# Kernel tuning notes

Measured on AMD Instinct MI355X. Metric: run time of the kernel, lower is better.

The kernel has to match this reference:

```python
import jax, jax.numpy as jnp
import numpy as np

D_MODEL = 1024
SEQ_LEN = 2048
NUM_EIGH = 24
BATCH = 4


def _spectral_filters(L, K):
    # Hankel matrix Z[i,j] = 2 / ((i+j)^3 - (i+j)), 1-indexed; top-K eigvecs scaled by sigma^0.25
    t = np.arange(1, L + 1, dtype=np.float64)
    s = t[:, None] + t[None, :]
    Z = 2.0 / (s ** 3 - s)
    sigma, phi = np.linalg.eigh(Z)
    phi_k = phi[:, -K:] * (sigma[-K:] ** 0.25)
    return jnp.asarray(phi_k, dtype=jnp.float32)


def setup_inputs() -> dict:
    key = jax.random.key(0)
    k1, k2, k3 = jax.random.split(key, 3)
    std = 1.0 / np.sqrt(D_MODEL)
    return {
        "x": jax.random.normal(k1, (BATCH, SEQ_LEN, D_MODEL), dtype=jnp.float32),
        "M_inputs": jax.random.normal(k2, (D_MODEL, D_MODEL), dtype=jnp.float32) * std,
        "M_filters": jax.random.normal(k3, (NUM_EIGH, D_MODEL), dtype=jnp.float32) * std,
        "phi": _spectral_filters(SEQ_LEN, NUM_EIGH),
    }


def _convolve_approx(u, v, n):
    # u: [B, L, D] inputs (already projected); v: [L, D] per-channel causal filters.
    # Dual-branch causal FFT convolution:
    #   plus[b,t,d]  = sum_{s<=t} v[s,d] * u[b,t-s,d]
    #   minus[b,t,d] = (-1)^t * sum_{s<=t} v[s,d] * (-1)^{t-s} u[b,t-s,d]
    B, L, D = u.shape
    sgn = jnp.where(jnp.arange(L) % 2 == 0, 1.0, -1.0).astype(u.dtype)[None, :, None]  # [1,L,1]
    V = jnp.fft.rfft(v, n=n, axis=0)                     # [F, D] complex
    U = jnp.stack([u, u * sgn], axis=-1)                 # [B, L, D, 2]
    Uf = jnp.fft.rfft(U, n=n, axis=1)                    # [B, F, D, 2]
    conv = jnp.fft.irfft(V[None, :, :, None] * Uf, n=n, axis=1)[:, :L]  # [B, L, D, 2]
    return conv[..., 0], conv[..., 1] * sgn


def reference(x, M_inputs, M_filters, phi):
    L = x.shape[1]
    n = 1 << int(np.ceil(np.log2(2 * L - 1)))  # next pow2 of 2L-1 (static)
    x_proj = x @ M_inputs                       # [B, L, D]
    phi_proj = phi[:L] @ M_filters              # [L, D]
    spectral_plus, spectral_minus = _convolve_approx(x_proj, phi_proj, n)
    return spectral_plus + spectral_minus
```

## Files before the change

### kernel.cpp

```cpp
#include <hip/hip_runtime.h>
#include <stdint.h>

#define D_MODEL 1024
#define SEQ 2048
#define HALF 1024
#define K_EIG 24
#define GUARD4 24
#define K4 128
#define K4P (GUARD4 + K4)
#define WE_JP4 72

typedef __attribute__((ext_vector_type(8))) short bf16x8;
typedef __attribute__((ext_vector_type(4))) float f32x4;
typedef _Float16 f16;
typedef _Float16 f16x2 __attribute__((ext_vector_type(2)));
typedef unsigned int uint;

#define GAS __attribute__((address_space(1)))
#define LAS __attribute__((address_space(3)))

static __device__ __forceinline__ unsigned short f2bf(float f) {
  union { float f; uint32_t u; } v; v.f = f;
  uint32_t u = v.u;
  u += 0x7FFFu + ((u >> 16) & 1u);
  return (unsigned short)(u >> 16);
}

static __device__ __forceinline__ float dot2(uint w2, uint u2, float c) {
  return __builtin_amdgcn_fdot2(__builtin_bit_cast(f16x2, w2),
                                __builtin_bit_cast(f16x2, u2), c, false);
}

static __device__ __forceinline__ uint pkrtz(float lo, float hi) {
  return __builtin_bit_cast(uint, __builtin_amdgcn_cvt_pkrtz(lo, hi));
}

static __device__ __forceinline__ uint pkbf(float lo, float hi) {
  return (uint)f2bf(lo) | ((uint)f2bf(hi) << 16);
}

__global__ __launch_bounds__(256) void k_prep(const float* __restrict__ Mi,
                                              const float* __restrict__ phi,
                                              const float* __restrict__ Mf,
                                              uint4* __restrict__ u4,
                                              unsigned short* __restrict__ Mt,
                                              uint4* __restrict__ we4) {
  __shared__ float smem[1056];
  const int blk = (int)blockIdx.x;
  const int tidx = threadIdx.x;

  if (blk < 768) {
    int r = blk / 96;
    int idx = (blk - r * 96) * 256 + tidx;
    u4[(size_t)r * (K4P * 1024) + idx] = make_uint4(0u, 0u, 0u, 0u);
    return;
  }
  if (blk < 1792) {
    int bidx = blk - 768;
    int n0 = (bidx & 31) * 32, k0 = (bidx >> 5) * 32;
    float (*tile)[33] = (float(*)[33])smem;
    int tx = tidx & 31, ty = tidx >> 5;
    #pragma unroll
    for (int r = 0; r < 32; r += 8)
      tile[ty + r][tx] = Mi[(size_t)(k0 + ty + r) * D_MODEL + n0 + tx];
    __syncthreads();
    #pragma unroll
    for (int r = 0; r < 32; r += 8)
      Mt[(size_t)(n0 + ty + r) * D_MODEL + k0 + tx] = f2bf(tile[tx][ty + r]);
    return;
  }
  {
    int bidx = blk - 1792;
    int jp4 = bidx % 72;
    int d = (bidx / 72) * 256 + tidx;
    if (jp4 >= 64) {
      we4[(size_t)jp4 * D_MODEL + d] = make_uint4(0u, 0u, 0u, 0u);
      return;
    }
    float (*ph)[K_EIG] = (float(*)[K_EIG])smem;
    if (tidx < 8 * K_EIG) {
      int s = tidx / K_EIG, k = tidx - s * K_EIG;
      ph[s][k] = phi[(size_t)(16 * jp4 + 2 * s) * K_EIG + k];
    }
    __syncthreads();
    float s[8] = {};
    #pragma unroll
    for (int k = 0; k < K_EIG; ++k) {
      float mv = Mf[(size_t)k * D_MODEL + d];
      #pragma unroll
      for (int j = 0; j < 8; ++j) s[j] = fmaf(ph[j][k], mv, s[j]);
    }
    uint4 o;
    o.x = pkrtz(2.f * s[0], 2.f * s[1]);
    o.y = pkrtz(2.f * s[2], 2.f * s[3]);
    o.z = pkrtz(2.f * s[4], 2.f * s[5]);
    o.w = pkrtz(2.f * s[6], 2.f * s[7]);
    we4[(size_t)jp4 * D_MODEL + d] = o;
  }
}

__global__ __launch_bounds__(256) void k_gemm(const float* __restrict__ X,
                                              const unsigned short* __restrict__ Bt,
                                              uint* __restrict__ Ug) {
  __shared__ float Asf[3][128 * 32];
  __shared__ unsigned short Bs[3][128 * 32];
  const int bid = (int)blockIdx.x;
  const int swz = (bid & 7) * 64 + (bid >> 3);
  const int m0 = (swz >> 3) * 128;
  const int n0 = (swz & 7) * 128;
  const int tid = threadIdx.x;
  const int lane = tid & 63;
  const int wave = tid >> 6;
  const int wm = wave >> 1, wn = wave & 1;
  const int qo = lane >> 4;

  const int a_row = lane >> 3;
  const int a_chunk = (lane & 7) ^ a_row;
  const int b_row = lane >> 2;
  const int b_chunk = (lane & 3) ^ (b_row & 3);

#define GSTAGE(buf, k0v)                                                                  \
  {                                                                                       \
    float* abase = &Asf[buf][0];                                                          \
    unsigned short* bbase = &Bs[buf][0];                                                  \
    _Pragma("unroll") for (int c = 0; c < 4; ++c) {                                       \
      int rbase = wave * 32 + c * 8;                                                      \
      const float* srcA = X + (size_t)(m0 + rbase + a_row) * 1024 + (k0v) + a_chunk * 4;  \
      __builtin_amdgcn_global_load_lds((const GAS void*)srcA,                             \
                                       (LAS void*)(abase + rbase * 32), 16, 0, 0);        \
    }                                                                                     \
    _Pragma("unroll") for (int c = 0; c < 2; ++c) {                                       \
      int rbase = wave * 32 + c * 16;                                                     \
      const unsigned short* srcB = Bt + (size_t)(n0 + rbase + b_row) * 1024 + (k0v) + b_chunk * 8; \
      __builtin_amdgcn_global_load_lds((const GAS void*)srcB,                             \
                                       (LAS void*)(bbase + rbase * 32), 16, 0, 0);        \
    }                                                                                     \
  }

  f32x4 acc[4][4] = {};

  GSTAGE(0, 0);
  GSTAGE(1, 32);

  int cur = 0;
  int nx2 = 2;
#pragma unroll 1
  for (int t = 0; t < 32; ++t) {
    if (t < 31) {
      asm volatile("s_waitcnt vmcnt(6)" ::: "memory");
    } else {
      asm volatile("s_waitcnt vmcnt(0)" ::: "memory");
    }
    __builtin_amdgcn_s_barrier();
    asm volatile("" ::: "memory");
    if (t < 30) GSTAGE(nx2, (t + 2) * 32);

    bf16x8 a[4], b[4];
    const float* Acur = &Asf[cur][0];
    const unsigned short* Bcur = &Bs[cur][0];
    #pragma unroll
    for (int mt = 0; mt < 4; ++mt) {
      int m = wm * 64 + mt * 16 + (lane & 15);
      const float* base = Acur + m * 32;
      int s0 = (2 * qo) ^ (lane & 7);
      int s1 = s0 ^ 1;
      float4 f0 = *(const float4*)(base + s0 * 4);
      float4 f1 = *(const float4*)(base + s1 * 4);
      uint4 pk;
      pk.x = pkbf(f0.x, f0.y); pk.y = pkbf(f0.z, f0.w);
      pk.z = pkbf(f1.x, f1.y); pk.w = pkbf(f1.z, f1.w);
      a[mt] = __builtin_bit_cast(bf16x8, pk);
    }
    #pragma unroll
    for (int nt = 0; nt < 4; ++nt) {
      int n = wn * 64 + nt * 16 + (lane & 15);
      int sb = qo ^ (lane & 3);
      b[nt] = *(const bf16x8*)(Bcur + n * 32 + sb * 8);
    }
    #pragma unroll
    for (int mt = 0; mt < 4; ++mt)
      #pragma unroll
      for (int nt = 0; nt < 4; ++nt)
        acc[mt][nt] = __builtin_amdgcn_mfma_f32_16x16x32_bf16(a[mt], b[nt], acc[mt][nt], 0, 0, 0);

    cur = (cur == 2) ? 0 : cur + 1;
    nx2 = (nx2 == 2) ? 0 : nx2 + 1;
  }
#undef GSTAGE

  const int crow = (lane >> 4) * 4;
  const int ccol = lane & 15;
  #pragma unroll
  for (int mt = 0; mt < 4; ++mt) {
    int m = m0 + wm * 64 + mt * 16 + crow;
    int b_ = m >> 11;
    int t0 = m & 2047;
    int r_e = b_ << 1;
    int k4 = t0 >> 4;
    int dwo = (t0 >> 2) & 3;
    size_t base_e = ((size_t)(r_e * K4P + GUARD4 + k4) * 1024) * 4 + dwo;
    size_t base_o = ((size_t)((r_e + 1) * K4P + GUARD4 + k4) * 1024) * 4 + dwo;
    #pragma unroll
    for (int nt = 0; nt < 4; ++nt) {
      int n = n0 + wn * 64 + nt * 16 + ccol;
      Ug[base_e + (size_t)n * 4] = pkrtz(acc[mt][nt][0], acc[mt][nt][2]);
      Ug[base_o + (size_t)n * 4] = pkrtz(acc[mt][nt][1], acc[mt][nt][3]);
    }
  }
}

__global__ __launch_bounds__(512, 6) void k_conv(const uint4* __restrict__ u4,
                                                 const uint4* __restrict__ we4,
                                                 float* __restrict__ out) {
  __shared__ uint4 u_r[32 * 64];
  __shared__ uint4 w_s[2][8][64];
  const int flat = blockIdx.x;
  const int dt = flat & 15;
  const int r  = (flat >> 4) & 7;
  const int a  = 7 - (flat >> 7);
  const int d0 = dt * 64;
  const int tid = threadIdx.x;
  const int dl = tid & 63;
  const int ig = tid >> 6;

  const uint4* ub = u4 + ((size_t)r * K4P + GUARD4) * 1024 + d0;
  const int b_ = r >> 1, p = r & 1;

#define STAGEU(k40)                                                                     \
  {                                                                                     \
    int k4e = (k40) + ig;                                                               \
    const uint4* src = ub + (long long)k4e * 1024 + dl;                                 \
    __builtin_amdgcn_global_load_lds((const GAS void*)src,                              \
                                     (LAS void*)(u_r + (k4e & 31) * 64), 16, 0, 0);     \
  }

#define STAGEW(ch)                                                                      \
  {                                                                                     \
    const uint4* src = we4 + (size_t)((ch) * 8 + ig) * 1024 + d0 + dl;                  \
    __builtin_amdgcn_global_load_lds((const GAS void*)src,                              \
                                     (LAS void*)(&w_s[(ch) & 1][ig][0]), 16, 0, 0);     \
  }

  const int i0 = a * 128;
  const int ibase = i0 + ig * 16;
  const int niter = (2 * a + 2) < 8 ? (2 * a + 2) : 8;

  STAGEU(16 * a - 8); STAGEU(16 * a); STAGEU(16 * a + 8);
  STAGEW(0);
  __syncthreads();

  float acc[16];
#pragma unroll
  for (int o = 0; o < 16; ++o) acc[o] = 0.f;

#pragma unroll 1
  for (int c = 0; c < niter; ++c) {
    STAGEU(16 * a - 8 * c - 16);
    STAGEW(c + 1);
    const int cb = c & 1;
    const int kbase = 16 * a + 2 * ig - 8 * c - 2;
#pragma unroll
    for (int s = 0; s < 4; ++s) {
      const int kb = kbase - 2 * s;
      uint4 v0 = u_r[((kb + 0) & 31) * 64 + dl];
      uint4 v1 = u_r[((kb + 1) & 31) * 64 + dl];
      uint4 v2 = u_r[((kb + 2) & 31) * 64 + dl];
      uint4 v3 = u_r[((kb + 3) & 31) * 64 + dl];
      uint P[16];
      P[0] = v0.x; P[1] = v0.y; P[2] = v0.z; P[3] = v0.w;
      P[4] = v1.x; P[5] = v1.y; P[6] = v1.z; P[7] = v1.w;
      P[8] = v2.x; P[9] = v2.y; P[10] = v2.z; P[11] = v2.w;
      P[12] = v3.x; P[13] = v3.y; P[14] = v3.z; P[15] = v3.w;
      uint4 wv0 = w_s[cb][2 * s][dl];
      uint4 wv1 = w_s[cb][2 * s + 1][dl];
      uint W[8];
      W[0] = wv0.x; W[1] = wv0.y; W[2] = wv0.z; W[3] = wv0.w;
      W[4] = wv1.x; W[5] = wv1.y; W[6] = wv1.z; W[7] = wv1.w;
      uint WS[8];
#pragma unroll
      for (int q = 0; q < 8; ++q) WS[q] = __builtin_amdgcn_alignbit(W[q], W[q], 16);
      uint pe[15];
#pragma unroll
      for (int j = 0; j < 15; ++j) pe[j] = __builtin_amdgcn_perm(P[j + 1], P[j], 0x03020504u);
#pragma unroll
      for (int q = 0; q < 8; ++q) {
#pragma unroll
        for (int h = 0; h < 8; ++h) {
          acc[2 * h]     = dot2(W[q],  pe[7 - q + h], acc[2 * h]);
          acc[2 * h + 1] = dot2(WS[q], P[8 - q + h],  acc[2 * h + 1]);
        }
      }
    }
    __syncthreads();
  }

#pragma unroll
  for (int o = 0; o < 16; ++o)
    out[((size_t)b_ * SEQ + 2 * (ibase + o) + p) * D_MODEL + d0 + dl] = acc[o];
#undef STAGEU
#undef STAGEW
}

extern "C" void kernel_launch(void* const* d_in, const int* in_sizes, int n_in,
                              void* d_out, int out_size, void* d_ws, size_t ws_size,
                              hipStream_t stream) {
  const float* x   = (const float*)d_in[0];
  const float* Mi  = (const float*)d_in[1];
  const float* Mf  = (const float*)d_in[2];
  const float* phi = (const float*)d_in[3];
  float* out = (float*)d_out;

  unsigned short* Mt = (unsigned short*)d_out;

  char* ws = (char*)d_ws;
  uint4* we4 = (uint4*)(ws);
  uint4* u4  = (uint4*)(ws + (2u << 20));

  hipLaunchKernelGGL(k_prep, dim3(2080), dim3(256), 0, stream, Mi, phi, Mf, u4, Mt, we4);
  hipLaunchKernelGGL(k_gemm, dim3(512), dim3(256), 0, stream, x, Mt, (uint*)u4);
  hipLaunchKernelGGL(k_conv, dim3(1024), dim3(512), 0, stream, u4, we4, out);
}
```

Baseline: 118.2 us.

## Load filter weights directly into registers with software prefetch instead of LDS

```diff
diff --git a/kernel.cpp b/kernel.cpp
--- a/kernel.cpp
+++ b/kernel.cpp
@@ -209,11 +209,10 @@
   }
 }
 
-__global__ __launch_bounds__(512, 6) void k_conv(const uint4* __restrict__ u4,
+__global__ __launch_bounds__(512, 8) void k_conv(const uint4* __restrict__ u4,
                                                  const uint4* __restrict__ we4,
                                                  float* __restrict__ out) {
   __shared__ uint4 u_r[32 * 64];
-  __shared__ uint4 w_s[2][8][64];
   const int flat = blockIdx.x;
   const int dt = flat & 15;
   const int r  = (flat >> 4) & 7;
@@ -224,6 +223,7 @@
   const int ig = tid >> 6;
 
   const uint4* ub = u4 + ((size_t)r * K4P + GUARD4) * 1024 + d0;
+  const uint4* wb = we4 + d0 + dl;
   const int b_ = r >> 1, p = r & 1;
 
 #define STAGEU(k40)                                                                     \
@@ -234,11 +234,33 @@
                                      (LAS void*)(u_r + (k4e & 31) * 64), 16, 0, 0);     \
   }
 
-#define STAGEW(ch)                                                                      \
+#define DOTS(kb_, wv0, wv1)                                                             \
   {                                                                                     \
-    const uint4* src = we4 + (size_t)((ch) * 8 + ig) * 1024 + d0 + dl;                  \
-    __builtin_amdgcn_global_load_lds((const GAS void*)src,                              \
-                                     (LAS void*)(&w_s[(ch) & 1][ig][0]), 16, 0, 0);     \
+    const int kb = (kb_);                                                               \
+    uint4 v0 = u_r[((kb + 0) & 31) * 64 + dl];                                          \
+    uint4 v1 = u_r[((kb + 1) & 31) * 64 + dl];                                          \
+    uint4 v2 = u_r[((kb + 2) & 31) * 64 + dl];                                          \
+    uint4 v3 = u_r[((kb + 3) & 31) * 64 + dl];                                          \
+    uint P[16];                                                                         \
+    P[0] = v0.x; P[1] = v0.y; P[2] = v0.z; P[3] = v0.w;                                 \
+    P[4] = v1.x; P[5] = v1.y; P[6] = v1.z; P[7] = v1.w;                                 \
+    P[8] = v2.x; P[9] = v2.y; P[10] = v2.z; P[11] = v2.w;                               \
+    P[12] = v3.x; P[13] = v3.y; P[14] = v3.z; P[15] = v3.w;                             \
+    uint W[8];                                                                          \
+    W[0] = (wv0).x; W[1] = (wv0).y; W[2] = (wv0).z; W[3] = (wv0).w;                     \
+    W[4] = (wv1).x; W[5] = (wv1).y; W[6] = (wv1).z; W[7] = (wv1).w;                     \
+    uint WS[8];                                                                         \
+    _Pragma("unroll") for (int q = 0; q < 8; ++q)                                       \
+      WS[q] = __builtin_amdgcn_alignbit(W[q], W[q], 16);                                \
+    uint pe[15];                                                                        \
+    _Pragma("unroll") for (int j = 0; j < 15; ++j)                                      \
+      pe[j] = __builtin_amdgcn_perm(P[j + 1], P[j], 0x03020504u);                       \
+    _Pragma("unroll") for (int q = 0; q < 8; ++q) {                                     \
+      _Pragma("unroll") for (int h = 0; h < 8; ++h) {                                   \
+        acc[2 * h]     = dot2(W[q],  pe[7 - q + h], acc[2 * h]);                        \
+        acc[2 * h + 1] = dot2(WS[q], P[8 - q + h],  acc[2 * h + 1]);                    \
+      }                                                                                 \
+    }                                                                                   \
   }
 
   const int i0 = a * 128;
@@ -246,51 +268,27 @@
   const int niter = (2 * a + 2) < 8 ? (2 * a + 2) : 8;
 
   STAGEU(16 * a - 8); STAGEU(16 * a); STAGEU(16 * a + 8);
-  STAGEW(0);
   __syncthreads();
 
   float acc[16];
 #pragma unroll
   for (int o = 0; o < 16; ++o) acc[o] = 0.f;
 
+  uint4 wA0 = wb[0], wA1 = wb[1024];
+  uint4 wB0, wB1;
+
 #pragma unroll 1
   for (int c = 0; c < niter; ++c) {
     STAGEU(16 * a - 8 * c - 16);
-    STAGEW(c + 1);
-    const int cb = c & 1;
     const int kbase = 16 * a + 2 * ig - 8 * c - 2;
-#pragma unroll
-    for (int s = 0; s < 4; ++s) {
-      const int kb = kbase - 2 * s;
-      uint4 v0 = u_r[((kb + 0) & 31) * 64 + dl];
-      uint4 v1 = u_r[((kb + 1) & 31) * 64 + dl];
-      uint4 v2 = u_r[((kb + 2) & 31) * 64 + dl];
-      uint4 v3 = u_r[((kb + 3) & 31) * 64 + dl];
-      uint P[16];
-      P[0] = v0.x; P[1] = v0.y; P[2] = v0.z; P[3] = v0.w;
-      P[4] = v1.x; P[5] = v1.y; P[6] = v1.z; P[7] = v1.w;
-      P[8] = v2.x; P[9] = v2.y; P[10] = v2.z; P[11] = v2.w;
-      P[12] = v3.x; P[13] = v3.y; P[14] = v3.z; P[15] = v3.w;
-      uint4 wv0 = w_s[cb][2 * s][dl];
-      uint4 wv1 = w_s[cb][2 * s + 1][dl];
-      uint W[8];
-      W[0] = wv0.x; W[1] = wv0.y; W[2] = wv0.z; W[3] = wv0.w;
-      W[4] = wv1.x; W[5] = wv1.y; W[6] = wv1.z; W[7] = wv1.w;
-      uint WS[8];
-#pragma unroll
-      for (int q = 0; q < 8; ++q) WS[q] = __builtin_amdgcn_alignbit(W[q], W[q], 16);
-      uint pe[15];
-#pragma unroll
-      for (int j = 0; j < 15; ++j) pe[j] = __builtin_amdgcn_perm(P[j + 1], P[j], 0x03020504u);
-#pragma unroll
-      for (int q = 0; q < 8; ++q) {
-#pragma unroll
-        for (int h = 0; h < 8; ++h) {
-          acc[2 * h]     = dot2(W[q],  pe[7 - q + h], acc[2 * h]);
-          acc[2 * h + 1] = dot2(WS[q], P[8 - q + h],  acc[2 * h + 1]);
-        }
-      }
-    }
+    wB0 = wb[(size_t)(8 * c + 2) * 1024]; wB1 = wb[(size_t)(8 * c + 3) * 1024];
+    DOTS(kbase - 0, wA0, wA1);
+    wA0 = wb[(size_t)(8 * c + 4) * 1024]; wA1 = wb[(size_t)(8 * c + 5) * 1024];
+    DOTS(kbase - 2, wB0, wB1);
+    wB0 = wb[(size_t)(8 * c + 6) * 1024]; wB1 = wb[(size_t)(8 * c + 7) * 1024];
+    DOTS(kbase - 4, wA0, wA1);
+    wA0 = wb[(size_t)(8 * c + 8) * 1024]; wA1 = wb[(size_t)(8 * c + 9) * 1024];
+    DOTS(kbase - 6, wB0, wB1);
     __syncthreads();
   }
 
@@ -298,7 +296,7 @@
   for (int o = 0; o < 16; ++o)
     out[((size_t)b_ * SEQ + 2 * (ibase + o) + p) * D_MODEL + d0 + dl] = acc[o];
 #undef STAGEU
-#undef STAGEW
+#undef DOTS
 }
 
 extern "C" void kernel_launch(void* const* d_in, const int* in_sizes, int n_in,
```

New measurement: 118.9 us. Within noise of the previous version (+0.6%).
